# Optimization experiments

Hardware: AMD Instinct MI355X
Metric: run time of the kernel (lower is better)

Reference implementation:

```python
import jax, jax.numpy as jnp
import numpy as np

B, N, DIM, K = 4, 4096, 128, 16


def setup_inputs() -> dict:
    key = jax.random.key(0)
    ks = jax.random.split(key, 20)
    s = 0.05
    inp = {
        "x": jax.random.normal(ks[0], (B, N, DIM), jnp.float32),
        "pos": jax.random.normal(ks[1], (B, N, 3), jnp.float32),
        # pos_mlp: Linear(3,dim) -> ReLU -> Linear(dim,dim)
        "pw1": jax.random.normal(ks[2], (3, DIM), jnp.float32) * s,
        "pb1": jnp.zeros((DIM,), jnp.float32),
        "pw2": jax.random.normal(ks[3], (DIM, DIM), jnp.float32) * s,
        "pb2": jnp.zeros((DIM,), jnp.float32),
        # q/k/v projections
        "qw": jax.random.normal(ks[4], (DIM, DIM), jnp.float32) * s,
        "qb": jnp.zeros((DIM,), jnp.float32),
        "kw": jax.random.normal(ks[5], (DIM, DIM), jnp.float32) * s,
        "kb": jnp.zeros((DIM,), jnp.float32),
        "vw": jax.random.normal(ks[6], (DIM, DIM), jnp.float32) * s,
        "vb": jnp.zeros((DIM,), jnp.float32),
        # attn MLP: Linear(dim, dim//4) -> ReLU -> Linear(dim//4, dim)
        "aw1": jax.random.normal(ks[7], (DIM, DIM // 4), jnp.float32) * s,
        "ab1": jnp.zeros((DIM // 4,), jnp.float32),
        "aw2": jax.random.normal(ks[8], (DIM // 4, DIM), jnp.float32) * s,
        "ab2": jnp.zeros((DIM,), jnp.float32),
    }
    return inp


def reference(x, pos, pw1, pb1, pw2, pb2, qw, qb, kw, kb, vw, vb, aw1, ab1, aw2, ab2):
    Bs, Np, C = x.shape
    k = K
    # pairwise squared distances: |pi|^2 + |pj|^2 - 2 pi.pj  -> (B,N,N)
    inner = jnp.einsum('bnd,bmd->bnm', pos, pos)
    xx = jnp.sum(pos * pos, axis=2, keepdims=True)  # (B,N,1)
    dist = xx + jnp.swapaxes(xx, 1, 2) - 2.0 * inner
    # k nearest neighbors (smallest dist) -> indices (B,N,k)
    _, idx = jax.lax.top_k(-dist, k)
    bidx = jnp.arange(Bs)[:, None, None]
    neighbors = x[bidx, idx]        # (B,N,k,C)
    pos_neighbors = pos[bidx, idx]  # (B,N,k,3)
    pos_relative = pos[:, :, None, :] - pos_neighbors  # (B,N,k,3)
    # pos MLP
    pe = jax.nn.relu(pos_relative @ pw1 + pb1) @ pw2 + pb2  # (B,N,k,C)
    q = (x @ qw + qb)[:, :, None, :]   # (B,N,1,C)
    kk = neighbors @ kw + kb           # (B,N,k,C)
    v = neighbors @ vw + vb            # (B,N,k,C)
    a = q - kk + pe
    attn = jax.nn.relu(a @ aw1 + ab1) @ aw2 + ab2  # (B,N,k,C)
    attn = jax.nn.softmax(attn, axis=2)
    out = jnp.sum(attn * (v + pe), axis=2)  # (B,N,C)
    return out
```

## Files before the change

kernel.cpp:

```cpp
#include <hip/hip_runtime.h>
#include <hip/hip_bf16.h>
#include <stdint.h>

#define BATCH 4
#define NPTS  4096
#define DIM   128
#define KNN   16
#define NROWS (BATCH*NPTS)
#define NCHUNK 16
#define CHUNK  (NPTS/NCHUNK)

typedef unsigned long long u64;
typedef unsigned int u32;
typedef unsigned short u16;
typedef __attribute__((ext_vector_type(8))) short short8;
typedef __attribute__((ext_vector_type(4))) float f32x4;

__device__ __forceinline__ u16 f2bf(float f) {
  u32 u = __float_as_uint(f);
  u += 0x7FFFu + ((u >> 16) & 1);
  return (u16)(u >> 16);
}

#define WAVE_LDS_FENCE() asm volatile("s_waitcnt lgkmcnt(0)" ::: "memory")

__global__ __launch_bounds__(256) void prep_all(
    const float* __restrict__ pos,
    const float* __restrict__ pw1, const float* __restrict__ pb1,
    const float* __restrict__ pw2, const float* __restrict__ pb2,
    const float* __restrict__ qw, const float* __restrict__ qb,
    const float* __restrict__ kw, const float* __restrict__ kb,
    const float* __restrict__ vw,
    const float* __restrict__ aw1, const float* __restrict__ ab1,
    const float* __restrict__ aw2,
    float4* __restrict__ pos4, u16* __restrict__ pw2T, u16* __restrict__ aw2T,
    u16* __restrict__ vwT, u16* __restrict__ w1T,
    u16* __restrict__ Wq2T, u16* __restrict__ Wk2T,
    float4* __restrict__ pw1q, float* __restrict__ bias1) {
  const int bid = blockIdx.x, tid = threadIdx.x;
  if (bid < 64) {
    int e = bid*256 + tid, k = e >> 7, n = e & 127;
    pw2T[n*128 + (k ^ ((n&7)<<3))] = f2bf(pw2[k*128 + n]);
  } else if (bid < 80) {
    int e = (bid-64)*256 + tid, k = e >> 7, n = e & 127;
    aw2T[n*32 + (k ^ ((n&3)<<3))] = f2bf(aw2[k*128 + n]);
  } else if (bid < 144) {
    int e = (bid-80)*256 + tid, k = e >> 7, n = e & 127;
    vwT[n*128 + (k ^ ((n&7)<<3))] = f2bf(vw[k*128 + n]);
  } else if (bid == 144) {
    if (tid < 128) {
      int c = tid;
      pw1q[c ^ ((c & 0x18) >> 2)] = make_float4(pw1[c], pw1[128+c], pw1[256+c], pb1[c]);
    } else if (tid < 160) {
      int j = tid - 128;
      float s = ab1[j];
      for (int c = 0; c < 128; ++c) s += (qb[c]-kb[c]+pb2[c]) * aw1[c*32+j];
      bias1[j] = s;
    }
  } else if (bid < 157) {
    int p = (bid-145) >> 2, qtr = (bid-145) & 3;
    const float* A = p == 0 ? pw2 : (p == 1 ? qw : kw);
    int j = tid & 31, r0 = qtr*32 + (tid >> 5)*4;
    float acc[4] = {0.f,0.f,0.f,0.f};
    for (int c = 0; c < 128; ++c) {
      float av = aw1[c*32 + j];
#pragma unroll
      for (int rr = 0; rr < 4; ++rr) acc[rr] = fmaf(A[(r0+rr)*128 + c], av, acc[rr]);
    }
#pragma unroll
    for (int rr = 0; rr < 4; ++rr) {
      int h = r0 + rr;
      u16 v = f2bf(acc[rr]);
      if (p == 0)      w1T [j*128 + (h ^ ((j&7)<<3))] = v;
      else if (p == 1) Wq2T[j*128 + (h ^ ((j&7)<<3))] = v;
      else             Wk2T[j*128 + (h ^ ((j&7)<<3))] = v;
    }
  } else {
    int i = (bid-157)*256 + tid;
    if (i < NROWS) pos4[i] = make_float4(pos[3*i], pos[3*i+1], pos[3*i+2], 0.f);
  }
}

template <typename T>
__device__ __forceinline__ void cex(T& a, T& b) {
  T mn = a < b ? a : b;
  T mx = a < b ? b : a;
  a = mn; b = mx;
}
template <typename T>
__device__ __forceinline__ void sort16(T x[16]) {
#pragma unroll
  for (int k = 2; k <= 16; k <<= 1)
#pragma unroll
    for (int j = k >> 1; j > 0; j >>= 1)
#pragma unroll
      for (int i = 0; i < 16; ++i) {
        int l = i ^ j;
        if (l > i) { if ((i & k) == 0) cex(x[i], x[l]); else cex(x[l], x[i]); }
      }
}
template <typename T>
__device__ __forceinline__ void merge16(T A[16], const T B[16]) {
#pragma unroll
  for (int i = 0; i < 16; ++i) { T b = B[15 - i]; A[i] = A[i] < b ? A[i] : b; }
#pragma unroll
  for (int j = 8; j > 0; j >>= 1)
#pragma unroll
    for (int i = 0; i < 16; ++i) { int l = i ^ j; if (l > i) cex(A[i], A[l]); }
}
__device__ __forceinline__ void bmerge32(u32 x[32]) {
#pragma unroll
  for (int j = 16; j > 0; j >>= 1)
#pragma unroll
    for (int i = 0; i < 32; ++i) { int l = i ^ j; if (l > i) cex(x[i], x[l]); }
}

__global__ __launch_bounds__(256) void knn_scan(const float4* __restrict__ pos4,
                                                u32* __restrict__ part) {
  __shared__ float4 cs[4][CHUNK];
  const int lane  = threadIdx.x & 63;
  const int w     = threadIdx.x >> 6;
  const int task  = blockIdx.x * 4 + w;
  const int qg    = task >> 4;
  const int chunk = task & 15;
  const int qbase = qg * 64;
  const int b     = qbase >> 12;
  const int cbase = chunk * CHUNK;

  const float4* cand = pos4 + b*NPTS + cbase;
#pragma unroll
  for (int i = 0; i < CHUNK/64; ++i) cs[w][lane + 64*i] = cand[lane + 64*i];
  __syncthreads();

  float4 qp = pos4[qbase + lane];
  const float qx = qp.x, qy = qp.y, qz = qp.z;

  u32 best[16];
#pragma unroll
  for (int i = 0; i < 16; ++i) best[i] = ~0u;

#pragma unroll 1
  for (int m = 0; m < CHUNK/16; ++m) {
    u32 batch[16];
#pragma unroll
    for (int e = 0; e < 16; ++e) {
      float4 p = cs[w][m*16 + e];
      float dx = qx - p.x, dy = qy - p.y, dz = qz - p.z;
      float d  = fmaf(dx, dx, fmaf(dy, dy, dz*dz));
      batch[e] = (__float_as_uint(d) & 0xFFFFF000u) | (u32)(cbase + m*16 + e);
    }
    u32 bmin = batch[0];
#pragma unroll
    for (int e = 1; e < 16; ++e) bmin = batch[e] < bmin ? batch[e] : bmin;
    if (__any(bmin < best[15])) {
      sort16(batch);
      merge16(best, batch);
    }
  }
  const int q = qbase + lane;
  uint4* dst = (uint4*)(part + q*256 + chunk*16);
#pragma unroll
  for (int t = 0; t < 4; ++t)
    dst[t] = make_uint4(best[4*t], best[4*t+1], best[4*t+2], best[4*t+3]);
}

__global__ __launch_bounds__(256) void knn_refine(const float4* __restrict__ pos4,
                                                  const u32* __restrict__ part,
                                                  int* __restrict__ knnIdx) {
  __shared__ u64 A64[16][137];
  __shared__ u32 Bu[16][264];
  u32 (*Au)[274] = (u32 (*)[274])A64;

  const int tid = threadIdx.x;
  const int qi = tid >> 4, c = tid & 15;
  const int q  = blockIdx.x * 16 + qi;
  const int b  = q >> 12;

  {
    const uint4* src = (const uint4*)(part + q*256 + c*16);
    u32 own[16];
#pragma unroll
    for (int t = 0; t < 4; ++t) {
      uint4 v = src[t];
      own[4*t+0]=v.x; own[4*t+1]=v.y; own[4*t+2]=v.z; own[4*t+3]=v.w;
    }
#pragma unroll
    for (int s = 0; s < 16; ++s) Au[qi][c*17 + s] = own[s];
  }
  __syncthreads();

  if (c < 8) {
    u32 x[32];
#pragma unroll
    for (int s = 0; s < 16; ++s) x[s]      = Au[qi][(2*c)*17 + s];
#pragma unroll
    for (int s = 0; s < 16; ++s) x[16 + s] = Au[qi][(2*c+1)*17 + 15 - s];
    bmerge32(x);
#pragma unroll
    for (int s = 0; s < 32; ++s) Bu[qi][c*33 + s] = x[s];
  }
  __syncthreads();

  if (c < 4) {
    u32 x[32];
#pragma unroll
    for (int s = 0; s < 32; ++s) {
      u32 a = Bu[qi][(2*c)*33 + s], bb = Bu[qi][(2*c+1)*33 + 31 - s];
      x[s] = a < bb ? a : bb;
    }
    bmerge32(x);
#pragma unroll
    for (int s = 0; s < 32; ++s) Au[qi][c*33 + s] = x[s];
  }
  __syncthreads();

  if (c < 2) {
    u32 x[32];
#pragma unroll
    for (int s = 0; s < 32; ++s) {
      u32 a = Au[qi][(2*c)*33 + s], bb = Au[qi][(2*c+1)*33 + 31 - s];
      x[s] = a < bb ? a : bb;
    }
    bmerge32(x);
#pragma unroll
    for (int s = 0; s < 32; ++s) Bu[qi][c*33 + s] = x[s];
  }
  __syncthreads();

  if (c == 0) {
    u32 x[32];
#pragma unroll
    for (int s = 0; s < 32; ++s) {
      u32 a = Bu[qi][s], bb = Bu[qi][33 + 31 - s];
      x[s] = a < bb ? a : bb;
    }
    bmerge32(x);
#pragma unroll
    for (int s = 0; s < 32; ++s) Bu[qi][132 + s] = x[s];
  }
  __syncthreads();

  if (c < 2) {
    float4 qp = pos4[q];
    const double qx = qp.x, qy = qp.y, qz = qp.z;
    u64 key[16];
#pragma unroll
    for (int s = 0; s < 16; ++s) {
      int idx = (int)(Bu[qi][132 + c*16 + s] & 0xFFFu);
      float4 p = pos4[(b<<12) + idx];
      double dx = qx - (double)p.x;
      double dy = qy - (double)p.y;
      double dz = qz - (double)p.z;
      double d  = fma(dx, dx, fma(dy, dy, dz*dz));
      key[s] = (((u64)__double_as_longlong(d)) & ~0xFFFull) | (u64)idx;
    }
    sort16(key);
#pragma unroll
    for (int s = 0; s < 16; ++s) A64[qi][c*17 + s] = key[s];
  }
  __syncthreads();

  if (c == 0) {
    u64 best[16], nb[16];
#pragma unroll
    for (int s = 0; s < 16; ++s) { best[s] = A64[qi][s]; nb[s] = A64[qi][17 + s]; }
    merge16(best, nb);
    const int outq = q * KNN;
#pragma unroll
    for (int s = 0; s < 16; ++s) knnIdx[outq + s] = (int)(best[s] & 0xFFFull);
  }
}

__global__ __launch_bounds__(256) void proj_mfma(
    const float* __restrict__ x, const u16* __restrict__ vwT,
    const u16* __restrict__ Wq2T, const u16* __restrict__ Wk2T,
    const float* __restrict__ vb,
    float* __restrict__ vo, float* __restrict__ qa, float* __restrict__ ka) {
  const int lane = threadIdx.x & 63, w = threadIdx.x >> 6;
  const int c16 = lane & 15, g = lane >> 4;
  const int row0 = (blockIdx.x*4 + w)*16;

  const float* xrow = x + (size_t)(row0 + c16)*DIM;
  short8 af[4];
#pragma unroll
  for (int kc = 0; kc < 4; ++kc) {
    float4 a0 = *(const float4*)&xrow[kc*32 + g*8];
    float4 a1 = *(const float4*)&xrow[kc*32 + g*8 + 4];
    short8 s;
    s[0]=(short)f2bf(a0.x); s[1]=(short)f2bf(a0.y); s[2]=(short)f2bf(a0.z); s[3]=(short)f2bf(a0.w);
    s[4]=(short)f2bf(a1.x); s[5]=(short)f2bf(a1.y); s[6]=(short)f2bf(a1.z); s[7]=(short)f2bf(a1.w);
    af[kc] = s;
  }

#pragma unroll
  for (int nt = 0; nt < 8; ++nt) {
    int n = nt*16 + c16;
    float bb = vb[n];
    f32x4 acc = {bb, bb, bb, bb};
#pragma unroll
    for (int kc = 0; kc < 4; ++kc) {
      short8 bf = *(const short8*)&vwT[n*128 + ((kc*32 + g*8) ^ ((n&7)<<3))];
      acc = __builtin_amdgcn_mfma_f32_16x16x32_bf16(af[kc], bf, acc, 0, 0, 0);
    }
#pragma unroll
    for (int r = 0; r < 4; ++r)
      vo[(size_t)(row0 + g*4 + r)*DIM + n] = acc[r];
  }

#pragma unroll
  for (int t = 0; t < 2; ++t) {
    int n = t*16 + c16;
    f32x4 aq = {0.f,0.f,0.f,0.f}, ak = {0.f,0.f,0.f,0.f};
#pragma unroll
    for (int kc = 0; kc < 4; ++kc) {
      short8 bq = *(const short8*)&Wq2T[n*128 + ((kc*32 + g*8) ^ ((n&7)<<3))];
      short8 bk = *(const short8*)&Wk2T[n*128 + ((kc*32 + g*8) ^ ((n&7)<<3))];
      aq = __builtin_amdgcn_mfma_f32_16x16x32_bf16(af[kc], bq, aq, 0, 0, 0);
      ak = __builtin_amdgcn_mfma_f32_16x16x32_bf16(af[kc], bk, ak, 0, 0, 0);
    }
#pragma unroll
    for (int r = 0; r < 4; ++r) {
      qa[(row0 + g*4 + r)*32 + n] = aq[r];
      ka[(row0 + g*4 + r)*32 + n] = ak[r];
    }
  }
}

__global__ __launch_bounds__(256, 4) void attn_mfma(
    const float4* __restrict__ pos4, const int* __restrict__ knnIdx,
    const float* __restrict__ vws, const float* __restrict__ qa, const float* __restrict__ ka,
    const u16* __restrict__ pw2T, const u16* __restrict__ w1T, const u16* __restrict__ aw2T,
    const float4* __restrict__ pw1q, const float* __restrict__ bias1,
    const float* __restrict__ pb2, const float* __restrict__ ab2,
    float* __restrict__ out) {
  __shared__ __align__(16) u16 pw2s[16384];
  __shared__ __align__(16) float4 pw1s[128];
  __shared__ float bias1s[32], pb2s[128], ab2s[128];
  __shared__ __align__(16) u16 h2t[4][512];

  const int tid = threadIdx.x;
  {
    const uint4* s1 = (const uint4*)pw2T; uint4* d1 = (uint4*)pw2s;
#pragma unroll
    for (int i = 0; i < 8; ++i) d1[tid + 256*i] = s1[tid + 256*i];
    if (tid < 128) { pw1s[tid] = pw1q[tid]; pb2s[tid] = pb2[tid]; ab2s[tid] = ab2[tid]; }
    else if (tid < 160) bias1s[tid-128] = bias1[tid-128];
  }
  __syncthreads();

  const int lane = tid & 63, w = tid >> 6;
  const int c16 = lane & 15, g = lane >> 4;

  const int swz = (blockIdx.x & 7) * 128 + (blockIdx.x >> 3);
  const int qblock = swz * 16;
  const int qbase  = qblock + w * 4;
  const int bofs   = (qblock >> 12) << 12;

  int id_own = knnIdx[qbase*KNN + lane];
  float4 pq = pos4[qbase + g];
  float4 pn = pos4[bofs + id_own];
  float rox = pq.x - pn.x, roy = pq.y - pn.y, roz = pq.z - pn.z;

#pragma unroll 1
  for (int j = 0; j < 4; ++j) {
    const int q = qbase + j;
    float relx = __shfl(rox, j*16 + c16);
    float rely = __shfl(roy, j*16 + c16);
    float relz = __shfl(roz, j*16 + c16);
    int idr[4];
#pragma unroll
    for (int r = 0; r < 4; ++r) idr[r] = __shfl(id_own, j*16 + g*4 + r);

    float qa_v[2], ka_v[2][4];
#pragma unroll
    for (int t = 0; t < 2; ++t) qa_v[t] = qa[q*32 + t*16 + c16];
#pragma unroll
    for (int r = 0; r < 4; ++r)
#pragma unroll
      for (int t = 0; t < 2; ++t) ka_v[t][r] = ka[(bofs + idr[r])*32 + t*16 + c16];

    short8 h1f[4];
#pragma unroll
    for (int kc = 0; kc < 4; ++kc) {
      short8 s;
#pragma unroll
      for (int jj = 0; jj < 8; ++jj) {
        int c = kc*32 + g*8 + jj;
        float4 wv = pw1s[c ^ ((c & 0x18) >> 2)];
        float h = fmaf(relx, wv.x, fmaf(rely, wv.y, fmaf(relz, wv.z, wv.w)));
        s[jj] = (short)f2bf(fmaxf(h, 0.f));
      }
      h1f[kc] = s;
    }

    f32x4 pe[8];
#pragma unroll
    for (int nt = 0; nt < 8; ++nt) { f32x4 z = {0.f,0.f,0.f,0.f}; pe[nt] = z; }
#pragma unroll
    for (int kc = 0; kc < 4; ++kc)
#pragma unroll
      for (int nt = 0; nt < 8; ++nt) {
        int n = nt*16 + c16;
        short8 bf = *(const short8*)&pw2s[n*128 + ((kc*32 + g*8) ^ ((n&7)<<3))];
        pe[nt] = __builtin_amdgcn_mfma_f32_16x16x32_bf16(h1f[kc], bf, pe[nt], 0, 0, 0);
      }

    f32x4 ha[2];
#pragma unroll
    for (int t = 0; t < 2; ++t) { f32x4 z = {0.f,0.f,0.f,0.f}; ha[t] = z; }
#pragma unroll
    for (int kc = 0; kc < 4; ++kc)
#pragma unroll
      for (int t = 0; t < 2; ++t) {
        int n = t*16 + c16;
        short8 bf = *(const short8*)&w1T[n*128 + ((kc*32 + g*8) ^ ((n&7)<<3))];
        ha[t] = __builtin_amdgcn_mfma_f32_16x16x32_bf16(h1f[kc], bf, ha[t], 0, 0, 0);
      }

#pragma unroll
    for (int t = 0; t < 2; ++t)
#pragma unroll
      for (int r = 0; r < 4; ++r) {
        float v = ha[t][r] + qa_v[t] - ka_v[t][r] + bias1s[t*16 + c16];
        int row = g*4 + r, col = t*16 + c16;
        h2t[w][row*32 + (col ^ ((row&3)<<3))] = f2bf(fmaxf(v, 0.f));
      }
    WAVE_LDS_FENCE();

    short8 h2f = *(const short8*)&h2t[w][c16*32 + ((g*8) ^ ((c16&3)<<3))];

#pragma unroll 1
    for (int nt = 0; nt < 8; ++nt) {
      float ab = ab2s[nt*16 + c16];
      f32x4 cini = {ab, ab, ab, ab};
      short8 baw = *(const short8*)&aw2T[(nt*16 + c16)*32 + ((g*8) ^ (((nt*16 + c16)&3)<<3))];
      f32x4 lg = __builtin_amdgcn_mfma_f32_16x16x32_bf16(h2f, baw, cini, 0, 0, 0);

      float m = fmaxf(fmaxf(lg[0], lg[1]), fmaxf(lg[2], lg[3]));
      m = fmaxf(m, __shfl_xor(m, 16));
      m = fmaxf(m, __shfl_xor(m, 32));
      float e0 = __expf(lg[0]-m), e1 = __expf(lg[1]-m),
            e2 = __expf(lg[2]-m), e3 = __expf(lg[3]-m);
      float s = e0+e1+e2+e3;
      s += __shfl_xor(s, 16);
      s += __shfl_xor(s, 32);
      float inv = 1.0f / s;
      float pb = pb2s[nt*16 + c16];
      float v0 = vws[(size_t)(bofs + idr[0])*DIM + nt*16 + c16];
      float v1 = vws[(size_t)(bofs + idr[1])*DIM + nt*16 + c16];
      float v2 = vws[(size_t)(bofs + idr[2])*DIM + nt*16 + c16];
      float v3 = vws[(size_t)(bofs + idr[3])*DIM + nt*16 + c16];
      float acc = e0*(v0 + pe[nt][0] + pb)
                + e1*(v1 + pe[nt][1] + pb)
                + e2*(v2 + pe[nt][2] + pb)
                + e3*(v3 + pe[nt][3] + pb);
      acc *= inv;
      acc += __shfl_xor(acc, 16);
      acc += __shfl_xor(acc, 32);
      if (lane < 16) out[q*DIM + nt*16 + lane] = acc;
    }
  }
}

extern "C" void kernel_launch(void* const* d_in, const int* in_sizes, int n_in,
                              void* d_out, int out_size, void* d_ws, size_t ws_size,
                              hipStream_t stream) {
  const float* x   = (const float*)d_in[0];
  const float* pos = (const float*)d_in[1];
  const float* pw1 = (const float*)d_in[2];
  const float* pb1 = (const float*)d_in[3];
  const float* pw2 = (const float*)d_in[4];
  const float* pb2 = (const float*)d_in[5];
  const float* qw  = (const float*)d_in[6];
  const float* qb  = (const float*)d_in[7];
  const float* kw  = (const float*)d_in[8];
  const float* kb  = (const float*)d_in[9];
  const float* vw  = (const float*)d_in[10];
  const float* vb  = (const float*)d_in[11];
  const float* aw1 = (const float*)d_in[12];
  const float* ab1 = (const float*)d_in[13];
  const float* aw2 = (const float*)d_in[14];
  const float* ab2 = (const float*)d_in[15];
  float* out = (float*)d_out;

  char* ws = (char*)d_ws;
  float4* pos4   = (float4*)(ws);
  int*    knnIdx = (int*)(ws + (1u<<20));
  u32*    part   = (u32*)(ws + (2u<<20));
  float*  vws    = (float*)(ws + (2u<<20));
  float*  qa     = (float*)(ws + (11u<<20));
  float*  ka     = (float*)(ws + (13u<<20));
  char*   wsw    = ws + (19u<<20);
  u16*    pw2T  = (u16*)(wsw);
  u16*    w1T   = (u16*)(wsw + 32768);
  u16*    aw2T  = (u16*)(wsw + 40960);
  u16*    vwT   = (u16*)(wsw + 49152);
  u16*    Wq2T  = (u16*)(wsw + 81920);
  u16*    Wk2T  = (u16*)(wsw + 90112);
  float4* pw1q  = (float4*)(wsw + 98304);
  float*  bias1 = (float*)(wsw + 100352);

  prep_all<<<221, 256, 0, stream>>>(pos, pw1, pb1, pw2, pb2, qw, qb, kw, kb, vw,
                                    aw1, ab1, aw2,
                                    pos4, pw2T, aw2T, vwT, w1T, Wq2T, Wk2T, pw1q, bias1);
  knn_scan<<<(NROWS/64)*NCHUNK/4, 256, 0, stream>>>(pos4, part);
  knn_refine<<<NROWS/16, 256, 0, stream>>>(pos4, part, knnIdx);
  proj_mfma<<<NROWS/64, 256, 0, stream>>>(x, vwT, Wq2T, Wk2T, vb, vws, qa, ka);
  attn_mfma<<<NROWS/16, 256, 0, stream>>>(pos4, knnIdx, vws, qa, ka,
                                          pw2T, w1T, aw2T, pw1q, bias1, pb2, ab2, out);
}
```

Measured before the change: 239.7 us.

## Fuse KNN scan and refine into one 1024-thread kernel using LDS

Merges the chunked KNN scan and the refine/merge kernel into a single kernel where 16 waves each scan one candidate chunk for 64 queries and write their partial top-16 lists to shared memory instead of global memory. The merge tree and double-precision re-ranking then run in the same block. This removes the global round-trip of the partial lists and one kernel launch. In exchange it uses large LDS (about 150KB) and 1024-thread blocks with only 256 blocks, which lowers occupancy and adds a block-wide barrier after the uneven-length scan phase.

Measured after the change: 232.9 us. 2.8% less time.

```diff
diff --git a/kernel.cpp b/kernel.cpp
--- a/kernel.cpp
+++ b/kernel.cpp
@@ -115,86 +115,67 @@
     for (int i = 0; i < 32; ++i) { int l = i ^ j; if (l > i) cex(x[i], x[l]); }
 }
 
-__global__ __launch_bounds__(256) void knn_scan(const float4* __restrict__ pos4,
-                                                u32* __restrict__ part) {
-  __shared__ float4 cs[4][CHUNK];
-  const int lane  = threadIdx.x & 63;
-  const int w     = threadIdx.x >> 6;
-  const int task  = blockIdx.x * 4 + w;
-  const int qg    = task >> 4;
-  const int chunk = task & 15;
-  const int qbase = qg * 64;
+__global__ __launch_bounds__(1024) void knn_all(const float4* __restrict__ pos4,
+                                                int* __restrict__ knnIdx) {
+  __shared__ __align__(16) u32 lists[64][273];
+  __shared__ __align__(16) u32 Bu[64][263];
+  __shared__ u64 rk[64][35];
+
+  const int tid  = threadIdx.x;
+  const int lane = tid & 63;
+  const int w    = tid >> 6;
+  const int qbase = blockIdx.x * 64;
   const int b     = qbase >> 12;
-  const int cbase = chunk * CHUNK;
-
-  const float4* cand = pos4 + b*NPTS + cbase;
-#pragma unroll
-  for (int i = 0; i < CHUNK/64; ++i) cs[w][lane + 64*i] = cand[lane + 64*i];
-  __syncthreads();
-
-  float4 qp = pos4[qbase + lane];
-  const float qx = qp.x, qy = qp.y, qz = qp.z;
-
-  u32 best[16];
-#pragma unroll
-  for (int i = 0; i < 16; ++i) best[i] = ~0u;
+  const int cbase = w * CHUNK;
+
+  {
+    float4* cs = (float4*)&Bu[0][0];
+    const float4* cand = pos4 + b*NPTS + cbase;
+#pragma unroll
+    for (int i = 0; i < CHUNK/64; ++i) cs[w*CHUNK + lane + 64*i] = cand[lane + 64*i];
+  }
+  WAVE_LDS_FENCE();
+
+  {
+    const float4* cs = (const float4*)&Bu[0][0];
+    float4 qp = pos4[qbase + lane];
+    const float qx = qp.x, qy = qp.y, qz = qp.z;
+
+    u32 best[16];
+#pragma unroll
+    for (int i = 0; i < 16; ++i) best[i] = ~0u;
 
 #pragma unroll 1
-  for (int m = 0; m < CHUNK/16; ++m) {
-    u32 batch[16];
-#pragma unroll
-    for (int e = 0; e < 16; ++e) {
-      float4 p = cs[w][m*16 + e];
-      float dx = qx - p.x, dy = qy - p.y, dz = qz - p.z;
-      float d  = fmaf(dx, dx, fmaf(dy, dy, dz*dz));
-      batch[e] = (__float_as_uint(d) & 0xFFFFF000u) | (u32)(cbase + m*16 + e);
-    }
-    u32 bmin = batch[0];
-#pragma unroll
-    for (int e = 1; e < 16; ++e) bmin = batch[e] < bmin ? batch[e] : bmin;
-    if (__any(bmin < best[15])) {
-      sort16(batch);
-      merge16(best, batch);
-    }
-  }
-  const int q = qbase + lane;
-  uint4* dst = (uint4*)(part + q*256 + chunk*16);
-#pragma unroll
-  for (int t = 0; t < 4; ++t)
-    dst[t] = make_uint4(best[4*t], best[4*t+1], best[4*t+2], best[4*t+3]);
-}
-
-__global__ __launch_bounds__(256) void knn_refine(const float4* __restrict__ pos4,
-                                                  const u32* __restrict__ part,
-                                                  int* __restrict__ knnIdx) {
-  __shared__ u64 A64[16][137];
-  __shared__ u32 Bu[16][264];
-  u32 (*Au)[274] = (u32 (*)[274])A64;
-
-  const int tid = threadIdx.x;
+    for (int m = 0; m < CHUNK/16; ++m) {
+      u32 batch[16];
+#pragma unroll
+      for (int e = 0; e < 16; ++e) {
+        float4 p = cs[w*CHUNK + m*16 + e];
+        float dx = qx - p.x, dy = qy - p.y, dz = qz - p.z;
+        float d  = fmaf(dx, dx, fmaf(dy, dy, dz*dz));
+        batch[e] = (__float_as_uint(d) & 0xFFFFF000u) | (u32)(cbase + m*16 + e);
+      }
+      u32 bmin = batch[0];
+#pragma unroll
+      for (int e = 1; e < 16; ++e) bmin = batch[e] < bmin ? batch[e] : bmin;
+      if (__any(bmin < best[15])) {
+        sort16(batch);
+        merge16(best, batch);
+      }
+    }
+#pragma unroll
+    for (int s = 0; s < 16; ++s) lists[lane][w*17 + s] = best[s];
+  }
+  __syncthreads();
+
   const int qi = tid >> 4, c = tid & 15;
-  const int q  = blockIdx.x * 16 + qi;
-  const int b  = q >> 12;
-
-  {
-    const uint4* src = (const uint4*)(part + q*256 + c*16);
-    u32 own[16];
-#pragma unroll
-    for (int t = 0; t < 4; ++t) {
-      uint4 v = src[t];
-      own[4*t+0]=v.x; own[4*t+1]=v.y; own[4*t+2]=v.z; own[4*t+3]=v.w;
-    }
-#pragma unroll
-    for (int s = 0; s < 16; ++s) Au[qi][c*17 + s] = own[s];
-  }
-  __syncthreads();
 
   if (c < 8) {
     u32 x[32];
 #pragma unroll
-    for (int s = 0; s < 16; ++s) x[s]      = Au[qi][(2*c)*17 + s];
-#pragma unroll
-    for (int s = 0; s < 16; ++s) x[16 + s] = Au[qi][(2*c+1)*17 + 15 - s];
+    for (int s = 0; s < 16; ++s) x[s]      = lists[qi][(2*c)*17 + s];
+#pragma unroll
+    for (int s = 0; s < 16; ++s) x[16 + s] = lists[qi][(2*c+1)*17 + 15 - s];
     bmerge32(x);
 #pragma unroll
     for (int s = 0; s < 32; ++s) Bu[qi][c*33 + s] = x[s];
@@ -210,7 +191,7 @@
     }
     bmerge32(x);
 #pragma unroll
-    for (int s = 0; s < 32; ++s) Au[qi][c*33 + s] = x[s];
+    for (int s = 0; s < 32; ++s) lists[qi][c*33 + s] = x[s];
   }
   __syncthreads();
 
@@ -218,7 +199,7 @@
     u32 x[32];
 #pragma unroll
     for (int s = 0; s < 32; ++s) {
-      u32 a = Au[qi][(2*c)*33 + s], bb = Au[qi][(2*c+1)*33 + 31 - s];
+      u32 a = lists[qi][(2*c)*33 + s], bb = lists[qi][(2*c+1)*33 + 31 - s];
       x[s] = a < bb ? a : bb;
     }
     bmerge32(x);
@@ -241,7 +222,7 @@
   __syncthreads();
 
   if (c < 2) {
-    float4 qp = pos4[q];
+    float4 qp = pos4[qbase + qi];
     const double qx = qp.x, qy = qp.y, qz = qp.z;
     u64 key[16];
 #pragma unroll
@@ -256,16 +237,16 @@
     }
     sort16(key);
 #pragma unroll
-    for (int s = 0; s < 16; ++s) A64[qi][c*17 + s] = key[s];
+    for (int s = 0; s < 16; ++s) rk[qi][c*17 + s] = key[s];
   }
   __syncthreads();
 
   if (c == 0) {
     u64 best[16], nb[16];
 #pragma unroll
-    for (int s = 0; s < 16; ++s) { best[s] = A64[qi][s]; nb[s] = A64[qi][17 + s]; }
+    for (int s = 0; s < 16; ++s) { best[s] = rk[qi][s]; nb[s] = rk[qi][17 + s]; }
     merge16(best, nb);
-    const int outq = q * KNN;
+    const int outq = (qbase + qi) * KNN;
 #pragma unroll
     for (int s = 0; s < 16; ++s) knnIdx[outq + s] = (int)(best[s] & 0xFFFull);
   }
@@ -486,7 +467,6 @@
   char* ws = (char*)d_ws;
   float4* pos4   = (float4*)(ws);
   int*    knnIdx = (int*)(ws + (1u<<20));
-  u32*    part   = (u32*)(ws + (2u<<20));
   float*  vws    = (float*)(ws + (2u<<20));
   float*  qa     = (float*)(ws + (11u<<20));
   float*  ka     = (float*)(ws + (13u<<20));
@@ -503,8 +483,7 @@
   prep_all<<<221, 256, 0, stream>>>(pos, pw1, pb1, pw2, pb2, qw, qb, kw, kb, vw,
                                     aw1, ab1, aw2,
                                     pos4, pw2T, aw2T, vwT, w1T, Wq2T, Wk2T, pw1q, bias1);
-  knn_scan<<<(NROWS/64)*NCHUNK/4, 256, 0, stream>>>(pos4, part);
-  knn_refine<<<NROWS/16, 256, 0, stream>>>(pos4, part, knnIdx);
+  knn_all<<<NROWS/64, 1024, 0, stream>>>(pos4, knnIdx);
   proj_mfma<<<NROWS/64, 256, 0, stream>>>(x, vwT, Wq2T, Wk2T, vb, vws, qa, ka);
   attn_mfma<<<NROWS/16, 256, 0, stream>>>(pos4, knnIdx, vws, qa, ka,
                                           pw2T, w1T, aw2T, pw1q, bias1, pb2, ab2, out);
```
